# Optimization experiments

Measured on AMD Instinct MI355X. Metric: run time of the kernel, lower is better.

The kernel has to match this reference:

```python
import jax, jax.numpy as jnp
import numpy as np

N = 8192          # total points (8 clouds x 1024)
B = 8             # number of point clouds
K = 64            # max_num_neighbors in radius()
R = 0.2           # ball radius
EPS = 1e-5        # BatchNorm eps


def _ball_query(pos, batch, r, k):
    # pos: [N,3], batch: [N] int. Returns (idx [N,k], valid [N,k]).
    d2 = jnp.sum((pos[:, None, :] - pos[None, :, :]) ** 2, axis=-1)  # [N,N]
    same = batch[:, None] == batch[None, :]
    ok = same & (d2 <= r * r)
    masked = jnp.where(ok, d2, jnp.inf)
    neg, idx = jax.lax.top_k(-masked, k)          # k nearest within ball
    valid = neg > -jnp.inf
    self_idx = jnp.arange(pos.shape[0])[:, None]
    idx = jnp.where(valid, idx, self_idx)          # pad invalid slots with self
    return idx, valid


def _mlp_layer(h, W, b, g, be, m, v):
    # Linear -> ReLU -> BatchNorm1d (eval mode, running stats)
    h = jax.nn.relu(h @ W + b)
    return g * (h - m) * jax.lax.rsqrt(v + EPS) + be


def setup_inputs() -> dict:
    key = jax.random.key(0)
    ks = jax.random.split(key, 8)
    x = jax.random.normal(ks[0], (N, 3), dtype=jnp.float32)
    pos = jax.random.uniform(ks[1], (N, 3), dtype=jnp.float32)
    batch = jnp.repeat(jnp.arange(B, dtype=jnp.int64), N // B)
    dims = [3, 64, 64, 128]
    params = {}
    for i in range(3):
        din, dout = dims[i], dims[i + 1]
        kw = jax.random.fold_in(ks[2], i)
        params[f"W{i+1}"] = jax.random.normal(kw, (din, dout), dtype=jnp.float32) / np.sqrt(din)
        params[f"b{i+1}"] = jnp.zeros((dout,), dtype=jnp.float32)
        params[f"g{i+1}"] = jnp.ones((dout,), dtype=jnp.float32)
        params[f"be{i+1}"] = jnp.zeros((dout,), dtype=jnp.float32)
        params[f"m{i+1}"] = jnp.zeros((dout,), dtype=jnp.float32)
        params[f"v{i+1}"] = jnp.ones((dout,), dtype=jnp.float32)
    return {"x": x, "pos": pos, "batch": batch, **params}


def reference(x, pos, batch,
              W1, b1, g1, be1, m1, v1,
              W2, b2, g2, be2, m2, v2,
              W3, b3, g3, be3, m3, v3):
    # radius ball query -> gather relative positions -> MLP([3,64,64,128]) -> max aggregation
    idx, valid = _ball_query(pos, batch, R, K)        # [N,K]
    rel = pos[idx] - pos[:, None, :]                   # [N,K,3]
    h = _mlp_layer(rel, W1, b1, g1, be1, m1, v1)       # [N,K,64]
    h = _mlp_layer(h, W2, b2, g2, be2, m2, v2)         # [N,K,64]
    h = _mlp_layer(h, W3, b3, g3, be3, m3, v3)         # [N,K,128]
    h = jnp.where(valid[:, :, None], h, -jnp.inf)
    mu = jnp.max(h, axis=1)                            # [N,128] (self edge always valid)
    return mu
```

## Files before the change

kernel.cpp:

```cpp
#include <hip/hip_runtime.h>
#include <stdint.h>

#define N_PTS 8192
#define SEG 1024

__device__ __forceinline__ float sq3(float dx, float dy, float dz) {
#pragma clang fp contract(off)
    float xx = dx * dx;
    float yy = dy * dy;
    float zz = dz * dz;
    return (xx + yy) + zz;
}

__device__ __forceinline__ float bcastf(float v, int k) {
    return __int_as_float(__builtin_amdgcn_readlane(__float_as_int(v), k));
}

__global__
__attribute__((amdgpu_flat_work_group_size(256, 256), amdgpu_waves_per_eu(1, 2)))
void sa_rl2(const float* __restrict__ pos,
            const float* __restrict__ W1, const float* __restrict__ b1,
            const float* __restrict__ g1, const float* __restrict__ be1,
            const float* __restrict__ m1, const float* __restrict__ v1,
            const float* __restrict__ W2, const float* __restrict__ b2,
            const float* __restrict__ g2, const float* __restrict__ be2,
            const float* __restrict__ m2, const float* __restrict__ v2,
            const float* __restrict__ W3, const float* __restrict__ b3,
            const float* __restrict__ g3, const float* __restrict__ be3,
            const float* __restrict__ m3, const float* __restrict__ v3,
            float* __restrict__ out, int* __restrict__ ctr)
{
    __shared__ float a1s[64], c1s[64], a2s[64], c2s[64];
    __shared__ int nbrs[4][64];

    const int tid  = threadIdx.x;
    const int lane = tid & 63;
    const int w    = tid >> 6;
    const int c    = lane;

    if (tid < 64) {
        float a1 = g1[tid] / sqrtf(v1[tid] + 1e-5f);
        a1s[tid] = a1;
        c1s[tid] = be1[tid] - m1[tid] * a1;
        float a2 = g2[tid] / sqrtf(v2[tid] + 1e-5f);
        a2s[tid] = a2;
        c2s[tid] = be2[tid] - m2[tid] * a2;
    }
    __syncthreads();

    const float w1x = W1[c], w1y = W1[64 + c], w1z = W1[128 + c];
    const float b1v = b1[c];

    float w2c[64];
    float b2c = b2[c];
#pragma unroll
    for (int k = 0; k < 64; ++k) {
        float wv = W2[k * 64 + c];
        w2c[k] = a1s[k] * wv;
        b2c = fmaf(c1s[k], wv, b2c);
    }

    float w3a[64], w3b[64];
    float b3a = b3[c], b3b = b3[64 + c];
#pragma unroll
    for (int k = 0; k < 64; ++k) {
        float wa = W3[k * 128 + c];
        float wb = W3[k * 128 + 64 + c];
        w3a[k] = a2s[k] * wa;
        w3b[k] = a2s[k] * wb;
        b3a = fmaf(c2s[k], wa, b3a);
        b3b = fmaf(c2s[k], wb, b3b);
    }

    const float a3a = g3[c] / sqrtf(v3[c] + 1e-5f);
    const float c3a = be3[c] - m3[c] * a3a;
    const float a3b = g3[64 + c] / sqrtf(v3[64 + c] + 1e-5f);
    const float c3b = be3[64 + c] - m3[64 + c] * a3b;

    const float R2 = (float)(0.2 * 0.2);
    const unsigned R2bits = __float_as_uint(R2);
    const unsigned long long below = (1ULL << lane) - 1ULL;

    for (;;) {
        int p0 = 0;
        if (lane == 0) p0 = atomicAdd(ctr, 1);
        const int p = __builtin_amdgcn_readfirstlane(p0);
        if (p >= N_PTS) break;

        const int base = p & ~(SEG - 1);
        const float px = pos[p * 3 + 0], py = pos[p * 3 + 1], pz = pos[p * 3 + 2];

        unsigned bits[16];
        int cnt = 0;
#pragma unroll
        for (int s = 0; s < 16; ++s) {
            int j = base + s * 64 + lane;
            float dx = pos[j * 3 + 0] - px;
            float dy = pos[j * 3 + 1] - py;
            float dz = pos[j * 3 + 2] - pz;
            float d2 = sq3(dx, dy, dz);
            bool ok = (d2 <= R2);
            bits[s] = ok ? __float_as_uint(d2) : 0xFFFFFFFFu;
            cnt += __popcll(__ballot(ok));
        }

        unsigned selm = 0;
        if (cnt <= 64) {
#pragma unroll
            for (int s = 0; s < 16; ++s)
                selm |= (bits[s] != 0xFFFFFFFFu ? 1u : 0u) << s;
        } else {
            unsigned lo = 0, hi = R2bits;
            while (lo < hi) {
                unsigned mid = lo + ((hi - lo) >> 1);
                int cc = 0;
#pragma unroll
                for (int s = 0; s < 16; ++s)
                    cc += __popcll(__ballot(bits[s] <= mid));
                if (cc >= 64) hi = mid; else lo = mid + 1;
            }
            const unsigned T = lo;
            int c1n = 0;
#pragma unroll
            for (int s = 0; s < 16; ++s)
                c1n += __popcll(__ballot(bits[s] < T));
            const int need = 64 - c1n;
            int eqbase = 0;
#pragma unroll
            for (int s = 0; s < 16; ++s) {
                unsigned long long em = __ballot(bits[s] == T);
                int rank = eqbase + __popcll(em & below);
                bool sel = (bits[s] < T) | ((bits[s] == T) & (rank < need));
                selm |= (sel ? 1u : 0u) << s;
                eqbase += __popcll(em);
            }
        }

        int nsel = 0;
#pragma unroll
        for (int s = 0; s < 16; ++s) {
            bool sel = (selm >> s) & 1u;
            unsigned long long m = __ballot(sel);
            int mypos = nsel + __popcll(m & below);
            if (sel) nbrs[w][mypos] = base + s * 64 + lane;
            nsel += __popcll(m);
        }
        asm volatile("s_waitcnt lgkmcnt(0)" ::: "memory");

        const int myj = (lane < nsel) ? nbrs[w][lane] : p;
        const float relx = pos[myj * 3 + 0] - px;
        const float rely = pos[myj * 3 + 1] - py;
        const float relz = pos[myj * 3 + 2] - pz;

        float mx0 = 0.f, mx1 = 0.f;
        for (int e = 0; e < nsel; ++e) {
            const float rx = bcastf(relx, e);
            const float ry = bcastf(rely, e);
            const float rz = bcastf(relz, e);

            const float h1 = fmaxf(fmaf(rx, w1x, fmaf(ry, w1y, fmaf(rz, w1z, b1v))), 0.f);

            float q0 = 0.f, q1 = 0.f, q2 = 0.f, q3 = 0.f;
#pragma unroll
            for (int k = 0; k < 64; k += 4) {
                q0 = fmaf(bcastf(h1, k + 0), w2c[k + 0], q0);
                q1 = fmaf(bcastf(h1, k + 1), w2c[k + 1], q1);
                q2 = fmaf(bcastf(h1, k + 2), w2c[k + 2], q2);
                q3 = fmaf(bcastf(h1, k + 3), w2c[k + 3], q3);
            }
            const float h2 = fmaxf(((q0 + q1) + (q2 + q3)) + b2c, 0.f);

            float r0 = 0.f, r1 = 0.f, s0 = 0.f, s1 = 0.f;
#pragma unroll
            for (int k = 0; k < 64; k += 2) {
                const float u0 = bcastf(h2, k);
                const float u1 = bcastf(h2, k + 1);
                r0 = fmaf(u0, w3a[k + 0], r0);  s0 = fmaf(u0, w3b[k + 0], s0);
                r1 = fmaf(u1, w3a[k + 1], r1);  s1 = fmaf(u1, w3b[k + 1], s1);
            }
            mx0 = fmaxf(mx0, (r0 + r1) + b3a);
            mx1 = fmaxf(mx1, (s0 + s1) + b3b);
        }

        out[p * 128 + c]      = fmaf(a3a, mx0, c3a);
        out[p * 128 + 64 + c] = fmaf(a3b, mx1, c3b);
    }
}

extern "C" void kernel_launch(void* const* d_in, const int* in_sizes, int n_in,
                              void* d_out, int out_size, void* d_ws, size_t ws_size,
                              hipStream_t stream) {
    const float* pos = (const float*)d_in[1];
    const float* W1 = (const float*)d_in[3];
    const float* b1 = (const float*)d_in[4];
    const float* g1 = (const float*)d_in[5];
    const float* be1 = (const float*)d_in[6];
    const float* m1 = (const float*)d_in[7];
    const float* v1 = (const float*)d_in[8];
    const float* W2 = (const float*)d_in[9];
    const float* b2 = (const float*)d_in[10];
    const float* g2 = (const float*)d_in[11];
    const float* be2 = (const float*)d_in[12];
    const float* m2 = (const float*)d_in[13];
    const float* v2 = (const float*)d_in[14];
    const float* W3 = (const float*)d_in[15];
    const float* b3 = (const float*)d_in[16];
    const float* g3 = (const float*)d_in[17];
    const float* be3 = (const float*)d_in[18];
    const float* m3 = (const float*)d_in[19];
    const float* v3 = (const float*)d_in[20];

    hipMemsetAsync(d_ws, 0, sizeof(int), stream);

    sa_rl2<<<512, 256, 0, stream>>>(pos,
                                    W1, b1, g1, be1, m1, v1,
                                    W2, b2, g2, be2, m2, v2,
                                    W3, b3, g3, be3, m3, v3,
                                    (float*)d_out, (int*)d_ws);
}
```

Before: 175.4 us.

## Stage folded MLP weights in swizzled LDS and batch 8 edges per pass

Moves the BN-folded W2 and W3 weights out of per-lane register arrays into XOR-swizzled shared memory and reads them as float4 with a one-step prefetch. Neighbor edges are now processed 8 at a time, so each weight load is reused across 8 edges. This lowers register pressure, which could allow more waves per SIMD, and amortizes weight traffic. In exchange it adds LDS reads and about 48KB of shared memory per block. Padded edges in a partial batch repeat the last valid neighbor, so the max result is unchanged.

```diff
diff --git a/kernel.cpp b/kernel.cpp
--- a/kernel.cpp
+++ b/kernel.cpp
@@ -3,6 +3,8 @@
 
 #define N_PTS 8192
 #define SEG 1024
+
+typedef __attribute__((ext_vector_type(4))) float f32x4;
 
 __device__ __forceinline__ float sq3(float dx, float dy, float dz) {
 #pragma clang fp contract(off)
@@ -16,9 +18,8 @@
     return __int_as_float(__builtin_amdgcn_readlane(__float_as_int(v), k));
 }
 
-__global__
-__attribute__((amdgpu_flat_work_group_size(256, 256), amdgpu_waves_per_eu(1, 2)))
-void sa_rl2(const float* __restrict__ pos,
+__global__ __launch_bounds__(256)
+void sa_lds(const float* __restrict__ pos,
             const float* __restrict__ W1, const float* __restrict__ b1,
             const float* __restrict__ g1, const float* __restrict__ be1,
             const float* __restrict__ m1, const float* __restrict__ v1,
@@ -31,6 +32,8 @@
             float* __restrict__ out, int* __restrict__ ctr)
 {
     __shared__ float a1s[64], c1s[64], a2s[64], c2s[64];
+    __shared__ __align__(16) float w2lds[64 * 64];
+    __shared__ __align__(16) float w3lds[64 * 128];
     __shared__ int nbrs[4][64];
 
     const int tid  = threadIdx.x;
@@ -48,34 +51,45 @@
     }
     __syncthreads();
 
+    for (int idx = tid; idx < 4096; idx += 256) {
+        int cc = idx & 63, k = idx >> 6;
+        float val = a1s[k] * W2[k * 64 + cc];
+        int phys = cc * 64 + ((((k >> 2) ^ (cc & 7)) << 2) | (k & 3));
+        w2lds[phys] = val;
+    }
+    for (int idx = tid; idx < 8192; idx += 256) {
+        int cc = idx & 63, f = idx >> 6;
+        int k = f >> 1, ab = f & 1;
+        float val = a2s[k] * W3[k * 128 + ab * 64 + cc];
+        int phys = cc * 128 + ((((k >> 1) ^ (cc & 7)) << 2) | ((k & 1) << 1) | ab);
+        w3lds[phys] = val;
+    }
+
     const float w1x = W1[c], w1y = W1[64 + c], w1z = W1[128 + c];
     const float b1v = b1[c];
 
-    float w2c[64];
     float b2c = b2[c];
-#pragma unroll
+#pragma unroll 8
+    for (int k = 0; k < 64; ++k) b2c = fmaf(c1s[k], W2[k * 64 + c], b2c);
+
+    float b3a = b3[c], b3b = b3[64 + c];
+#pragma unroll 8
     for (int k = 0; k < 64; ++k) {
-        float wv = W2[k * 64 + c];
-        w2c[k] = a1s[k] * wv;
-        b2c = fmaf(c1s[k], wv, b2c);
-    }
-
-    float w3a[64], w3b[64];
-    float b3a = b3[c], b3b = b3[64 + c];
-#pragma unroll
-    for (int k = 0; k < 64; ++k) {
-        float wa = W3[k * 128 + c];
-        float wb = W3[k * 128 + 64 + c];
-        w3a[k] = a2s[k] * wa;
-        w3b[k] = a2s[k] * wb;
-        b3a = fmaf(c2s[k], wa, b3a);
-        b3b = fmaf(c2s[k], wb, b3b);
+        b3a = fmaf(c2s[k], W3[k * 128 + c], b3a);
+        b3b = fmaf(c2s[k], W3[k * 128 + 64 + c], b3b);
     }
 
     const float a3a = g3[c] / sqrtf(v3[c] + 1e-5f);
     const float c3a = be3[c] - m3[c] * a3a;
     const float a3b = g3[64 + c] / sqrtf(v3[64 + c] + 1e-5f);
     const float c3b = be3[64 + c] - m3[64 + c] * a3b;
+
+    __syncthreads();
+
+    const int sbase2 = c * 256 + ((c & 7) << 4);
+    const int sbase3 = c * 512 + ((c & 7) << 4);
+    const char* w2p = (const char*)w2lds;
+    const char* w3p = (const char*)w3lds;
 
     const float R2 = (float)(0.2 * 0.2);
     const unsigned R2bits = __float_as_uint(R2);
@@ -153,33 +167,60 @@
         const float relz = pos[myj * 3 + 2] - pz;
 
         float mx0 = 0.f, mx1 = 0.f;
-        for (int e = 0; e < nsel; ++e) {
-            const float rx = bcastf(relx, e);
-            const float ry = bcastf(rely, e);
-            const float rz = bcastf(relz, e);
-
-            const float h1 = fmaxf(fmaf(rx, w1x, fmaf(ry, w1y, fmaf(rz, w1z, b1v))), 0.f);
-
-            float q0 = 0.f, q1 = 0.f, q2 = 0.f, q3 = 0.f;
-#pragma unroll
-            for (int k = 0; k < 64; k += 4) {
-                q0 = fmaf(bcastf(h1, k + 0), w2c[k + 0], q0);
-                q1 = fmaf(bcastf(h1, k + 1), w2c[k + 1], q1);
-                q2 = fmaf(bcastf(h1, k + 2), w2c[k + 2], q2);
-                q3 = fmaf(bcastf(h1, k + 3), w2c[k + 3], q3);
-            }
-            const float h2 = fmaxf(((q0 + q1) + (q2 + q3)) + b2c, 0.f);
-
-            float r0 = 0.f, r1 = 0.f, s0 = 0.f, s1 = 0.f;
-#pragma unroll
-            for (int k = 0; k < 64; k += 2) {
-                const float u0 = bcastf(h2, k);
-                const float u1 = bcastf(h2, k + 1);
-                r0 = fmaf(u0, w3a[k + 0], r0);  s0 = fmaf(u0, w3b[k + 0], s0);
-                r1 = fmaf(u1, w3a[k + 1], r1);  s1 = fmaf(u1, w3b[k + 1], s1);
-            }
-            mx0 = fmaxf(mx0, (r0 + r1) + b3a);
-            mx1 = fmaxf(mx1, (s0 + s1) + b3b);
+        const int nb = (nsel + 7) >> 3;
+        for (int bb = 0; bb < nb; ++bb) {
+            const int eb = bb * 8;
+
+            float h1v[8];
+#pragma unroll
+            for (int j = 0; j < 8; ++j) {
+                int ej = eb + j;  ej = (ej < nsel) ? ej : (nsel - 1);
+                float rx = bcastf(relx, ej);
+                float ry = bcastf(rely, ej);
+                float rz = bcastf(relz, ej);
+                h1v[j] = fmaxf(fmaf(rx, w1x, fmaf(ry, w1y, fmaf(rz, w1z, b1v))), 0.f);
+            }
+
+            float z2v[8];
+#pragma unroll
+            for (int j = 0; j < 8; ++j) z2v[j] = b2c;
+            f32x4 wv = *(const f32x4*)(w2p + (sbase2 ^ 0));
+            for (int g = 0; g < 16; ++g) {
+                f32x4 wn = *(const f32x4*)(w2p + (sbase2 ^ (((g + 1) & 15) << 4)));
+#pragma unroll
+                for (int kk = 0; kk < 4; ++kk) {
+                    const int k = g * 4 + kk;
+#pragma unroll
+                    for (int j = 0; j < 8; ++j)
+                        z2v[j] = fmaf(bcastf(h1v[j], k), wv[kk], z2v[j]);
+                }
+                wv = wn;
+            }
+            float h2v[8];
+#pragma unroll
+            for (int j = 0; j < 8; ++j) h2v[j] = fmaxf(z2v[j], 0.f);
+
+            float rv[8], sv[8];
+#pragma unroll
+            for (int j = 0; j < 8; ++j) { rv[j] = 0.f; sv[j] = 0.f; }
+            f32x4 w3v = *(const f32x4*)(w3p + (sbase3 ^ 0));
+            for (int p2 = 0; p2 < 32; ++p2) {
+                f32x4 w3n = *(const f32x4*)(w3p + (sbase3 ^ (((p2 + 1) & 31) << 4)));
+                const int k0 = p2 * 2;
+#pragma unroll
+                for (int j = 0; j < 8; ++j) {
+                    float u0 = bcastf(h2v[j], k0);
+                    float u1 = bcastf(h2v[j], k0 + 1);
+                    rv[j] = fmaf(u0, w3v[0], rv[j]);  sv[j] = fmaf(u0, w3v[1], sv[j]);
+                    rv[j] = fmaf(u1, w3v[2], rv[j]);  sv[j] = fmaf(u1, w3v[3], sv[j]);
+                }
+                w3v = w3n;
+            }
+            float mr = rv[0], ms = sv[0];
+#pragma unroll
+            for (int j = 1; j < 8; ++j) { mr = fmaxf(mr, rv[j]); ms = fmaxf(ms, sv[j]); }
+            mx0 = fmaxf(mx0, mr + b3a);
+            mx1 = fmaxf(mx1, ms + b3b);
         }
 
         out[p * 128 + c]      = fmaf(a3a, mx0, c3a);
@@ -212,7 +253,7 @@
 
     hipMemsetAsync(d_ws, 0, sizeof(int), stream);
 
-    sa_rl2<<<512, 256, 0, stream>>>(pos,
+    sa_lds<<<512, 256, 0, stream>>>(pos,
                                     W1, b1, g1, be1, m1, v1,
                                     W2, b2, g2, be2, m2, v2,
                                     W3, b3, g3, be3, m3, v3,
```

Result: slower. 244.3 us (+39.3%).

## Process four neighbor edges per MLP pass and move half of W3 to LDS

Applied to the files above, without the earlier changes.

The per-edge MLP loop now handles four neighbor edges at once. Each weight register or LDS load is reused across four independent FMA chains, which adds instruction-level parallelism. The second half of the folded W3 weights moves from registers to shared memory to free VGPRs for the wider batch, and launch bounds are set to 256x2. Padding edges duplicate the last valid neighbor, so the max is unchanged. The cost is extra LDS reads per k and some wasted work when the neighbor count is not a multiple of four.

```diff
diff --git a/kernel.cpp b/kernel.cpp
--- a/kernel.cpp
+++ b/kernel.cpp
@@ -16,21 +16,21 @@
     return __int_as_float(__builtin_amdgcn_readlane(__float_as_int(v), k));
 }
 
-__global__
-__attribute__((amdgpu_flat_work_group_size(256, 256), amdgpu_waves_per_eu(1, 2)))
-void sa_rl2(const float* __restrict__ pos,
-            const float* __restrict__ W1, const float* __restrict__ b1,
-            const float* __restrict__ g1, const float* __restrict__ be1,
-            const float* __restrict__ m1, const float* __restrict__ v1,
-            const float* __restrict__ W2, const float* __restrict__ b2,
-            const float* __restrict__ g2, const float* __restrict__ be2,
-            const float* __restrict__ m2, const float* __restrict__ v2,
-            const float* __restrict__ W3, const float* __restrict__ b3,
-            const float* __restrict__ g3, const float* __restrict__ be3,
-            const float* __restrict__ m3, const float* __restrict__ v3,
-            float* __restrict__ out, int* __restrict__ ctr)
+__global__ __launch_bounds__(256, 2)
+void sa_v2(const float* __restrict__ pos,
+           const float* __restrict__ W1, const float* __restrict__ b1,
+           const float* __restrict__ g1, const float* __restrict__ be1,
+           const float* __restrict__ m1, const float* __restrict__ v1,
+           const float* __restrict__ W2, const float* __restrict__ b2,
+           const float* __restrict__ g2, const float* __restrict__ be2,
+           const float* __restrict__ m2, const float* __restrict__ v2,
+           const float* __restrict__ W3, const float* __restrict__ b3,
+           const float* __restrict__ g3, const float* __restrict__ be3,
+           const float* __restrict__ m3, const float* __restrict__ v3,
+           float* __restrict__ out, int* __restrict__ ctr)
 {
     __shared__ float a1s[64], c1s[64], a2s[64], c2s[64];
+    __shared__ float w3b_lds[64 * 64];
     __shared__ int nbrs[4][64];
 
     const int tid  = threadIdx.x;
@@ -48,6 +48,11 @@
     }
     __syncthreads();
 
+    for (int idx = tid; idx < 4096; idx += 256) {
+        int cc = idx & 63, k = idx >> 6;
+        w3b_lds[k * 64 + cc] = a2s[k] * W3[k * 128 + 64 + cc];
+    }
+
     const float w1x = W1[c], w1y = W1[64 + c], w1z = W1[128 + c];
     const float b1v = b1[c];
 
@@ -60,22 +65,22 @@
         b2c = fmaf(c1s[k], wv, b2c);
     }
 
-    float w3a[64], w3b[64];
+    float w3a[64];
     float b3a = b3[c], b3b = b3[64 + c];
 #pragma unroll
     for (int k = 0; k < 64; ++k) {
         float wa = W3[k * 128 + c];
-        float wb = W3[k * 128 + 64 + c];
         w3a[k] = a2s[k] * wa;
-        w3b[k] = a2s[k] * wb;
         b3a = fmaf(c2s[k], wa, b3a);
-        b3b = fmaf(c2s[k], wb, b3b);
+        b3b = fmaf(c2s[k], W3[k * 128 + 64 + c], b3b);
     }
 
     const float a3a = g3[c] / sqrtf(v3[c] + 1e-5f);
     const float c3a = be3[c] - m3[c] * a3a;
     const float a3b = g3[64 + c] / sqrtf(v3[64 + c] + 1e-5f);
     const float c3b = be3[64 + c] - m3[64 + c] * a3b;
+
+    __syncthreads();
 
     const float R2 = (float)(0.2 * 0.2);
     const unsigned R2bits = __float_as_uint(R2);
@@ -153,33 +158,47 @@
         const float relz = pos[myj * 3 + 2] - pz;
 
         float mx0 = 0.f, mx1 = 0.f;
-        for (int e = 0; e < nsel; ++e) {
-            const float rx = bcastf(relx, e);
-            const float ry = bcastf(rely, e);
-            const float rz = bcastf(relz, e);
-
-            const float h1 = fmaxf(fmaf(rx, w1x, fmaf(ry, w1y, fmaf(rz, w1z, b1v))), 0.f);
-
-            float q0 = 0.f, q1 = 0.f, q2 = 0.f, q3 = 0.f;
-#pragma unroll
-            for (int k = 0; k < 64; k += 4) {
-                q0 = fmaf(bcastf(h1, k + 0), w2c[k + 0], q0);
-                q1 = fmaf(bcastf(h1, k + 1), w2c[k + 1], q1);
-                q2 = fmaf(bcastf(h1, k + 2), w2c[k + 2], q2);
-                q3 = fmaf(bcastf(h1, k + 3), w2c[k + 3], q3);
-            }
-            const float h2 = fmaxf(((q0 + q1) + (q2 + q3)) + b2c, 0.f);
-
-            float r0 = 0.f, r1 = 0.f, s0 = 0.f, s1 = 0.f;
-#pragma unroll
-            for (int k = 0; k < 64; k += 2) {
-                const float u0 = bcastf(h2, k);
-                const float u1 = bcastf(h2, k + 1);
-                r0 = fmaf(u0, w3a[k + 0], r0);  s0 = fmaf(u0, w3b[k + 0], s0);
-                r1 = fmaf(u1, w3a[k + 1], r1);  s1 = fmaf(u1, w3b[k + 1], s1);
-            }
-            mx0 = fmaxf(mx0, (r0 + r1) + b3a);
-            mx1 = fmaxf(mx1, (s0 + s1) + b3b);
+        const int nb = (nsel + 3) >> 2;
+        for (int bb = 0; bb < nb; ++bb) {
+            const int eb = bb * 4;
+
+            float h1v[4];
+#pragma unroll
+            for (int j = 0; j < 4; ++j) {
+                int ej = eb + j;  ej = (ej < nsel) ? ej : (nsel - 1);
+                float rx = bcastf(relx, ej);
+                float ry = bcastf(rely, ej);
+                float rz = bcastf(relz, ej);
+                h1v[j] = fmaxf(fmaf(rx, w1x, fmaf(ry, w1y, fmaf(rz, w1z, b1v))), 0.f);
+            }
+
+            float z2v[4] = {b2c, b2c, b2c, b2c};
+#pragma unroll
+            for (int k = 0; k < 64; ++k) {
+#pragma unroll
+                for (int j = 0; j < 4; ++j)
+                    z2v[j] = fmaf(bcastf(h1v[j], k), w2c[k], z2v[j]);
+            }
+            float h2v[4];
+#pragma unroll
+            for (int j = 0; j < 4; ++j) h2v[j] = fmaxf(z2v[j], 0.f);
+
+            float rv[4] = {0.f, 0.f, 0.f, 0.f};
+            float sv[4] = {0.f, 0.f, 0.f, 0.f};
+#pragma unroll
+            for (int k = 0; k < 64; ++k) {
+                const float wbk = w3b_lds[k * 64 + c];
+#pragma unroll
+                for (int j = 0; j < 4; ++j) {
+                    const float u = bcastf(h2v[j], k);
+                    rv[j] = fmaf(u, w3a[k], rv[j]);
+                    sv[j] = fmaf(u, wbk,   sv[j]);
+                }
+            }
+            float mr = fmaxf(fmaxf(rv[0], rv[1]), fmaxf(rv[2], rv[3]));
+            float ms = fmaxf(fmaxf(sv[0], sv[1]), fmaxf(sv[2], sv[3]));
+            mx0 = fmaxf(mx0, mr + b3a);
+            mx1 = fmaxf(mx1, ms + b3b);
         }
 
         out[p * 128 + c]      = fmaf(a3a, mx0, c3a);
@@ -212,9 +231,9 @@
 
     hipMemsetAsync(d_ws, 0, sizeof(int), stream);
 
-    sa_rl2<<<512, 256, 0, stream>>>(pos,
-                                    W1, b1, g1, be1, m1, v1,
-                                    W2, b2, g2, be2, m2, v2,
-                                    W3, b3, g3, be3, m3, v3,
-                                    (float*)d_out, (int*)d_ws);
-}
+    sa_v2<<<512, 256, 0, stream>>>(pos,
+                                   W1, b1, g1, be1, m1, v1,
+                                   W2, b2, g2, be2, m2, v2,
+                                   W3, b3, g3, be3, m3, v3,
+                                   (float*)d_out, (int*)d_ws);
+}
```

Result: slower. 201.8 us (+15.1%).
